# Kernel optimization log

Hardware: AMD Instinct MI355X
Metric: run time of the kernel (lower is better)

The kernel has to match this reference:

```python
import jax, jax.numpy as jnp
import numpy as np

N, E, D = 40000, 640000, 128
EPS = 1e-5


def _lin(k, out_d, in_d):
    s = 1.0 / np.sqrt(in_d)
    kw, kb = jax.random.split(k)
    W = jax.random.uniform(kw, (out_d, in_d), minval=-s, maxval=s, dtype=jnp.float32)
    b = jax.random.uniform(kb, (out_d,), minval=-s, maxval=s, dtype=jnp.float32)
    return W, b


def setup_inputs() -> dict:
    key = jax.random.key(0)
    kx, ke, k1, k2, k3, k4 = jax.random.split(key, 6)
    x = jax.random.normal(kx, (N, D), dtype=jnp.float32)
    edge_index = jax.random.randint(ke, (2, E), 0, N, dtype=jnp.int64)
    Wm1, bm1 = _lin(k1, D, D)
    Wm2, bm2 = _lin(k2, D, D)
    Wu1, bu1 = _lin(k3, D, 2 * D)
    Wu2, bu2 = _lin(k4, D, D)
    gamma = jnp.ones((D,), jnp.float32)
    beta = jnp.zeros((D,), jnp.float32)
    return dict(x=x, edge_index=edge_index, Wm1=Wm1, bm1=bm1, Wm2=Wm2, bm2=bm2,
                Wu1=Wu1, bu1=bu1, Wu2=Wu2, bu2=bu2, gamma=gamma, beta=beta)


def reference(x, edge_index, Wm1, bm1, Wm2, bm2, Wu1, bu1, Wu2, bu2, gamma, beta):
    num_nodes = x.shape[0]
    src, dst = edge_index[0], edge_index[1]
    # message MLP on gathered source features: (E, D)
    m = jax.nn.relu(x[src] @ Wm1.T + bm1) @ Wm2.T + bm2
    # scatter-mean via segment_sum + clamped count
    agg = jax.ops.segment_sum(m, dst, num_segments=num_nodes)
    cnt = jax.ops.segment_sum(jnp.ones((dst.shape[0],), m.dtype), dst, num_segments=num_nodes)
    agg = agg / jnp.clip(cnt, 1.0, None)[:, None]
    # update MLP on concat([x, agg]) -> (N, D); dropout is identity in eval
    comb = jnp.concatenate([x, agg], axis=-1)
    u = jax.nn.relu(comb @ Wu1.T + bu1) @ Wu2.T + bu2
    # residual + LayerNorm
    h = u + x
    mu = h.mean(-1, keepdims=True)
    var = ((h - mu) ** 2).mean(-1, keepdims=True)
    return (h - mu) / jnp.sqrt(var + EPS) * gamma + beta
```

## Files before the change

kernel.cpp:

```cpp
#include <hip/hip_runtime.h>

#define N_NODES 40000
#define N_EDGES 640000
#define DIM 128
#define PAD 64
#define NBLK_GEMM 313

typedef __bf16 bf16;
typedef __bf16 v8bf __attribute__((ext_vector_type(8)));
typedef __bf16 v4bf __attribute__((ext_vector_type(4)));
typedef float f32x4 __attribute__((ext_vector_type(4)));

#define MFMA(a, b, c) __builtin_amdgcn_mfma_f32_16x16x32_bf16(a, b, c, 0, 0, 0)

#define OFF_WM1 0
#define OFF_BM1 16384
#define OFF_WM2 16512
#define OFF_BM2 32896
#define OFF_WU1 33024
#define OFF_BU1 65792
#define OFF_WU2 65920
#define OFF_BU2 82304
#define OFF_GAM 82432
#define OFF_BET 82560
#define NPARAM  82688

__global__ __launch_bounds__(256) void front_kernel(
    const void* __restrict__ x, const void* __restrict__ ei,
    const void* p0, const void* p1, const void* p2, const void* p3,
    const void* p4, const void* p5, const void* p6, const void* p7,
    const void* p8, const void* p9,
    bf16* __restrict__ wp, bf16* __restrict__ xb,
    int* __restrict__ cnt, int* __restrict__ flags)
{
    __shared__ int sf[2];
    const int tid = threadIdx.x;
    const int gid = blockIdx.x * 256 + tid;
    const int gstride = gridDim.x * 256;

    if (tid == 0) { sf[0] = 0; sf[1] = 0; }
    __syncthreads();
    {
        const unsigned short* xh = (const unsigned short*)x;
        const unsigned int* eiw = (const unsigned int*)ei;
        int isf32 = 0; unsigned int orhi = 0;
        #pragma unroll
        for (int j = 0; j < 4; ++j) {
            unsigned short h = xh[2 * (tid + 256 * j)];
            if (((h >> 7) & 0xFF) >= 0xC0) isf32 = 1;
            orhi |= eiw[2 * (tid + 256 * j) + 1];
        }
        if (isf32) atomicOr(&sf[0], 1);
        if (orhi)  atomicOr(&sf[1], 1);
    }
    __syncthreads();
    const int f32m = sf[0];
    if (blockIdx.x == 0 && tid == 0) { flags[0] = f32m; flags[1] = sf[1] ? 0 : 1; }

    for (int i = gid; i < NPARAM; i += gstride) {
        const void* src; int base;
        if      (i < OFF_BM1) { src = p0; base = OFF_WM1; }
        else if (i < OFF_WM2) { src = p1; base = OFF_BM1; }
        else if (i < OFF_BM2) { src = p2; base = OFF_WM2; }
        else if (i < OFF_WU1) { src = p3; base = OFF_BM2; }
        else if (i < OFF_BU1) { src = p4; base = OFF_WU1; }
        else if (i < OFF_WU2) { src = p5; base = OFF_BU1; }
        else if (i < OFF_BU2) { src = p6; base = OFF_WU2; }
        else if (i < OFF_GAM) { src = p7; base = OFF_BU2; }
        else if (i < OFF_BET) { src = p8; base = OFF_GAM; }
        else                  { src = p9; base = OFF_BET; }
        int j = i - base;
        float v = f32m ? ((const float*)src)[j] : (float)((const bf16*)src)[j];
        wp[i] = (bf16)v;
    }
    {
        const int NT = N_NODES * DIM;
        if (f32m) {
            const float4* g = (const float4*)x;
            v4bf* o = (v4bf*)xb;
            for (int i = gid; i < NT / 4; i += gstride) {
                float4 v = g[i];
                v4bf t; t[0] = (bf16)v.x; t[1] = (bf16)v.y; t[2] = (bf16)v.z; t[3] = (bf16)v.w;
                o[i] = t;
            }
        } else {
            const uint4* g = (const uint4*)x;
            uint4* o = (uint4*)xb;
            for (int i = gid; i < NT / 8; i += gstride) o[i] = g[i];
        }
    }
    for (int i = gid; i < N_NODES; i += gstride) cnt[i] = 0;
}

__global__ __launch_bounds__(256) void scatter_kernel(const void* __restrict__ ei,
                                                      int* __restrict__ cnt,
                                                      int* __restrict__ padded,
                                                      const int* __restrict__ flags) {
    int e = blockIdx.x * 256 + threadIdx.x;
    if (e >= N_EDGES) return;
    int s, d;
    if (flags[1]) {
        const long long* p = (const long long*)ei;
        s = (int)p[e]; d = (int)p[N_EDGES + e];
    } else {
        const int* p = (const int*)ei;
        s = p[e]; d = p[N_EDGES + e];
    }
    int pos = atomicAdd(&cnt[d], 1);
    if (pos < PAD) padded[(d << 6) + pos] = s;
}

__global__ __launch_bounds__(256) void msg_kernel(const bf16* __restrict__ xb,
                                                  const bf16* __restrict__ wp,
                                                  bf16* __restrict__ y)
{
    __shared__ __align__(16) bf16 sc[4][32 * DIM];
    const int wave = threadIdx.x >> 6, lane = threadIdx.x & 63;
    const int l15 = lane & 15, quad = lane >> 4;
    const int row0 = (blockIdx.x * 4 + wave) * 32;
    bf16* s = sc[wave];
    const bf16* W1 = wp + OFF_WM1;
    const bf16* W2 = wp + OFF_WM2;

    const int ra = min(row0 + l15, N_NODES - 1);
    const int rb = min(row0 + 16 + l15, N_NODES - 1);

    f32x4 acc[2][8] = {};
    #pragma unroll
    for (int kt = 0; kt < 4; ++kt) {
        int k0 = kt * 32 + quad * 8;
        v8bf a0 = *(const v8bf*)&xb[(size_t)ra * DIM + k0];
        v8bf a1 = *(const v8bf*)&xb[(size_t)rb * DIM + k0];
        #pragma unroll
        for (int ct = 0; ct < 8; ++ct) {
            v8bf b = *(const v8bf*)&W1[(ct * 16 + l15) * DIM + k0];
            acc[0][ct] = MFMA(a0, b, acc[0][ct]);
            acc[1][ct] = MFMA(a1, b, acc[1][ct]);
        }
    }
    #pragma unroll
    for (int ct = 0; ct < 8; ++ct) {
        float bb = (float)wp[OFF_BM1 + ct * 16 + l15];
        int c8w = (ct << 1) | (l15 >> 3);
        #pragma unroll
        for (int i = 0; i < 2; ++i)
            #pragma unroll
            for (int r = 0; r < 4; ++r) {
                int row = i * 16 + quad * 4 + r;
                s[row * DIM + (((c8w ^ (row & 15)) << 3) | (l15 & 7))] =
                    (bf16)fmaxf(acc[i][ct][r] + bb, 0.f);
            }
    }
    f32x4 acc2[2][8] = {};
    #pragma unroll
    for (int kt = 0; kt < 4; ++kt) {
        int k0 = kt * 32 + quad * 8;
        int c8 = kt * 4 + quad;
        v8bf a0 = *(const v8bf*)&s[l15 * DIM + ((c8 ^ l15) << 3)];
        v8bf a1 = *(const v8bf*)&s[(16 + l15) * DIM + ((c8 ^ l15) << 3)];
        #pragma unroll
        for (int ct = 0; ct < 8; ++ct) {
            v8bf b = *(const v8bf*)&W2[(ct * 16 + l15) * DIM + k0];
            acc2[0][ct] = MFMA(a0, b, acc2[0][ct]);
            acc2[1][ct] = MFMA(a1, b, acc2[1][ct]);
        }
    }
    #pragma unroll
    for (int ct = 0; ct < 8; ++ct) {
        float bb = (float)wp[OFF_BM2 + ct * 16 + l15];
        #pragma unroll
        for (int i = 0; i < 2; ++i)
            #pragma unroll
            for (int r = 0; r < 4; ++r) {
                int grow = row0 + i * 16 + quad * 4 + r;
                if (grow < N_NODES)
                    y[(size_t)grow * DIM + ct * 16 + l15] = (bf16)(acc2[i][ct][r] + bb);
            }
    }
}

__global__ __launch_bounds__(256) void update_kernel(const bf16* __restrict__ xb,
                                                     const bf16* __restrict__ agg,
                                                     const bf16* __restrict__ wp,
                                                     const int* __restrict__ flags,
                                                     void* __restrict__ out)
{
    __shared__ __align__(16) bf16 sc[4][32 * DIM];
    const int wave = threadIdx.x >> 6, lane = threadIdx.x & 63;
    const int l15 = lane & 15, quad = lane >> 4;
    const int row0 = (blockIdx.x * 4 + wave) * 32;
    bf16* s = sc[wave];
    const bf16* W1 = wp + OFF_WU1;
    const bf16* W2 = wp + OFF_WU2;
    const int of32 = flags[0];

    const int ra = min(row0 + l15, N_NODES - 1);
    const int rb = min(row0 + 16 + l15, N_NODES - 1);

    f32x4 acc[2][8] = {};
    #pragma unroll
    for (int kt = 0; kt < 8; ++kt) {
        int k0 = kt * 32 + quad * 8;
        const bf16* A = (kt < 4) ? xb : agg;
        int ko = (kt < 4) ? k0 : (k0 - 128);
        v8bf a0 = *(const v8bf*)&A[(size_t)ra * DIM + ko];
        v8bf a1 = *(const v8bf*)&A[(size_t)rb * DIM + ko];
        #pragma unroll
        for (int ct = 0; ct < 8; ++ct) {
            v8bf b = *(const v8bf*)&W1[(ct * 16 + l15) * 256 + k0];
            acc[0][ct] = MFMA(a0, b, acc[0][ct]);
            acc[1][ct] = MFMA(a1, b, acc[1][ct]);
        }
    }
    #pragma unroll
    for (int ct = 0; ct < 8; ++ct) {
        float bb = (float)wp[OFF_BU1 + ct * 16 + l15];
        int c8w = (ct << 1) | (l15 >> 3);
        #pragma unroll
        for (int i = 0; i < 2; ++i)
            #pragma unroll
            for (int r = 0; r < 4; ++r) {
                int row = i * 16 + quad * 4 + r;
                s[row * DIM + (((c8w ^ (row & 15)) << 3) | (l15 & 7))] =
                    (bf16)fmaxf(acc[i][ct][r] + bb, 0.f);
            }
    }
    f32x4 acc2[2][8] = {};
    #pragma unroll
    for (int kt = 0; kt < 4; ++kt) {
        int k0 = kt * 32 + quad * 8;
        int c8 = kt * 4 + quad;
        v8bf a0 = *(const v8bf*)&s[l15 * DIM + ((c8 ^ l15) << 3)];
        v8bf a1 = *(const v8bf*)&s[(16 + l15) * DIM + ((c8 ^ l15) << 3)];
        #pragma unroll
        for (int ct = 0; ct < 8; ++ct) {
            v8bf b = *(const v8bf*)&W2[(ct * 16 + l15) * DIM + k0];
            acc2[0][ct] = MFMA(a0, b, acc2[0][ct]);
            acc2[1][ct] = MFMA(a1, b, acc2[1][ct]);
        }
    }

    float bu2c[8], gc[8], bc[8];
    #pragma unroll
    for (int ct = 0; ct < 8; ++ct) {
        int col = ct * 16 + l15;
        bu2c[ct] = (float)wp[OFF_BU2 + col];
        gc[ct]   = (float)wp[OFF_GAM + col];
        bc[ct]   = (float)wp[OFF_BET + col];
    }
    #pragma unroll
    for (int i = 0; i < 2; ++i) {
        #pragma unroll
        for (int r = 0; r < 4; ++r) {
            int grow = row0 + i * 16 + quad * 4 + r;
            int growc = min(grow, N_NODES - 1);
            float u[8], s1 = 0.f, s2 = 0.f;
            #pragma unroll
            for (int ct = 0; ct < 8; ++ct) {
                float v = acc2[i][ct][r] + bu2c[ct]
                        + (float)xb[(size_t)growc * DIM + ct * 16 + l15];
                u[ct] = v; s1 += v; s2 += v * v;
            }
            #pragma unroll
            for (int off = 1; off < 16; off <<= 1) {
                s1 += __shfl_xor(s1, off);
                s2 += __shfl_xor(s2, off);
            }
            float mean = s1 * (1.f / 128.f);
            float var  = s2 * (1.f / 128.f) - mean * mean;
            float rstd = rsqrtf(var + 1e-5f);
            if (grow < N_NODES) {
                if (of32) {
                    #pragma unroll
                    for (int ct = 0; ct < 8; ++ct)
                        ((float*)out)[(size_t)grow * DIM + ct * 16 + l15] =
                            (u[ct] - mean) * rstd * gc[ct] + bc[ct];
                } else {
                    #pragma unroll
                    for (int ct = 0; ct < 8; ++ct)
                        ((bf16*)out)[(size_t)grow * DIM + ct * 16 + l15] =
                            (bf16)((u[ct] - mean) * rstd * gc[ct] + bc[ct]);
                }
            }
        }
    }
}

__device__ __forceinline__ void accum8(float* s, uint4 v) {
    v8bf b = __builtin_bit_cast(v8bf, v);
    #pragma unroll
    for (int j = 0; j < 8; ++j) s[j] += (float)b[j];
}

__global__ __launch_bounds__(256) void agg_kernel(const bf16* __restrict__ y,
                                                  const int* __restrict__ padded,
                                                  const int* __restrict__ cnt,
                                                  bf16* __restrict__ agg) {
    const int node = (blockIdx.x << 2) + (threadIdx.x >> 6);
    const int lane = threadIdx.x & 63;
    const int slot = lane >> 4, c16 = lane & 15;
    const int c = min(cnt[node], PAD);
    const int beg = node << 6;
    const int end = beg + c;
    const uint4* yv = (const uint4*)y;

    float s0[8] = {}, s1[8] = {};
    int e = beg + slot;
    for (; e + 4 < end; e += 8) {
        int i0 = padded[e], i1 = padded[e + 4];
        uint4 v0 = yv[(size_t)i0 * 16 + c16];
        uint4 v1 = yv[(size_t)i1 * 16 + c16];
        accum8(s0, v0);
        accum8(s1, v1);
    }
    if (e < end) accum8(s0, yv[(size_t)padded[e] * 16 + c16]);

    float inv = 1.f / (float)(c > 0 ? c : 1);
    v8bf o;
    #pragma unroll
    for (int j = 0; j < 8; ++j) {
        float v = s0[j] + s1[j];
        v += __shfl_xor(v, 16);
        v += __shfl_xor(v, 32);
        o[j] = (bf16)(v * inv);
    }
    if (slot == 0)
        ((uint4*)agg)[(size_t)node * 16 + c16] = __builtin_bit_cast(uint4, o);
}

extern "C" void kernel_launch(void* const* d_in, const int* in_sizes, int n_in,
                              void* d_out, int out_size, void* d_ws, size_t ws_size,
                              hipStream_t stream) {
    const void* x  = d_in[0];
    const void* ei = d_in[1];

    char* ws = (char*)d_ws;
    size_t off = 0;
    auto alloc = [&](size_t bytes) {
        void* p = ws + off;
        off += (bytes + 255) & ~(size_t)255;
        return p;
    };
    bf16* y      = (bf16*)alloc((size_t)N_NODES * DIM * sizeof(bf16));
    bf16* agg    = (bf16*)alloc((size_t)N_NODES * DIM * sizeof(bf16));
    bf16* xb     = (bf16*)alloc((size_t)N_NODES * DIM * sizeof(bf16));
    bf16* wp     = (bf16*)alloc((size_t)NPARAM * sizeof(bf16));
    int*  cnt    = (int*)alloc(N_NODES * sizeof(int));
    int*  padded = (int*)alloc((size_t)N_NODES * PAD * sizeof(int));
    int*  flags  = (int*)alloc(256);

    front_kernel<<<1024, 256, 0, stream>>>(
        x, ei, d_in[2], d_in[3], d_in[4], d_in[5], d_in[6], d_in[7],
        d_in[8], d_in[9], d_in[10], d_in[11], wp, xb, cnt, flags);
    scatter_kernel<<<(N_EDGES + 255) / 256, 256, 0, stream>>>(ei, cnt, padded, flags);
    msg_kernel<<<NBLK_GEMM, 256, 0, stream>>>(xb, wp, y);
    agg_kernel<<<N_NODES / 4, 256, 0, stream>>>(y, padded, cnt, agg);
    update_kernel<<<NBLK_GEMM, 256, 0, stream>>>(xb, agg, wp, flags, d_out);
}
```

Measured before the change: 221.3 us.

## Fuse conversion into scatter, shrink GEMM tiles, use 16-bit neighbor indices

Merges the front conversion kernel into the scatter kernel, with each thread handling four edges for more atomic-level parallelism, and replaces the counter zeroing with a memset. Neighbor indices are stored as 16-bit values to halve padded-list traffic. The message and update GEMM kernels now give each wave 16 rows instead of 32, doubling the grid to 625 blocks for better occupancy at the cost of reusing weight loads less. Node ids up to 40000 fit in unsigned short, but the memset is now a separate launch and the tail bounds checks were removed because 40000 divides evenly.

Result: slower. 227.5 us (+2.8%).

```diff
diff --git a/kernel.cpp b/kernel.cpp
--- a/kernel.cpp
+++ b/kernel.cpp
@@ -4,7 +4,9 @@
 #define N_EDGES 640000
 #define DIM 128
 #define PAD 64
-#define NBLK_GEMM 313
+#define NBLK_GEMM 625
+#define SCAT_ILP 4
+#define SCAT_BLOCKS (N_EDGES / (256 * SCAT_ILP))
 
 typedef __bf16 bf16;
 typedef __bf16 v8bf __attribute__((ext_vector_type(8)));
@@ -25,38 +27,79 @@
 #define OFF_BET 82560
 #define NPARAM  82688
 
-__global__ __launch_bounds__(256) void front_kernel(
+__device__ __forceinline__ void detect(const void* x, const void* ei,
+                                       int* sf, int& f32m, int& i64m) {
+    const int tid = threadIdx.x;
+    if (tid == 0) { sf[0] = 0; sf[1] = 0; }
+    __syncthreads();
+    const unsigned short* xh = (const unsigned short*)x;
+    const unsigned int* eiw = (const unsigned int*)ei;
+    int isf32 = 0; unsigned int orhi = 0;
+    #pragma unroll
+    for (int j = 0; j < 4; ++j) {
+        unsigned short h = xh[2 * (tid + 256 * j)];
+        if (((h >> 7) & 0xFF) >= 0xC0) isf32 = 1;
+        orhi |= eiw[2 * (tid + 256 * j) + 1];
+    }
+    if (isf32) atomicOr(&sf[0], 1);
+    if (orhi)  atomicOr(&sf[1], 1);
+    __syncthreads();
+    f32m = sf[0];
+    i64m = sf[1] ? 0 : 1;
+}
+
+__global__ __launch_bounds__(256) void scatter_kernel(
     const void* __restrict__ x, const void* __restrict__ ei,
     const void* p0, const void* p1, const void* p2, const void* p3,
     const void* p4, const void* p5, const void* p6, const void* p7,
     const void* p8, const void* p9,
-    bf16* __restrict__ wp, bf16* __restrict__ xb,
-    int* __restrict__ cnt, int* __restrict__ flags)
+    int* __restrict__ cnt, unsigned short* __restrict__ padded,
+    bf16* __restrict__ xb, bf16* __restrict__ wp, int* __restrict__ flags)
 {
     __shared__ int sf[2];
-    const int tid = threadIdx.x;
-    const int gid = blockIdx.x * 256 + tid;
-    const int gstride = gridDim.x * 256;
-
-    if (tid == 0) { sf[0] = 0; sf[1] = 0; }
-    __syncthreads();
-    {
-        const unsigned short* xh = (const unsigned short*)x;
-        const unsigned int* eiw = (const unsigned int*)ei;
-        int isf32 = 0; unsigned int orhi = 0;
-        #pragma unroll
-        for (int j = 0; j < 4; ++j) {
-            unsigned short h = xh[2 * (tid + 256 * j)];
-            if (((h >> 7) & 0xFF) >= 0xC0) isf32 = 1;
-            orhi |= eiw[2 * (tid + 256 * j) + 1];
-        }
-        if (isf32) atomicOr(&sf[0], 1);
-        if (orhi)  atomicOr(&sf[1], 1);
-    }
-    __syncthreads();
-    const int f32m = sf[0];
-    if (blockIdx.x == 0 && tid == 0) { flags[0] = f32m; flags[1] = sf[1] ? 0 : 1; }
-
+    int f32m, i64m;
+    detect(x, ei, sf, f32m, i64m);
+    const int gid = blockIdx.x * 256 + threadIdx.x;
+    const int gstride = SCAT_BLOCKS * 256;
+    if (gid == 0) { flags[0] = f32m; flags[1] = i64m; }
+
+    int s[SCAT_ILP], d[SCAT_ILP];
+    if (i64m) {
+        const long long* p = (const long long*)ei;
+        #pragma unroll
+        for (int j = 0; j < SCAT_ILP; ++j) {
+            int e = gid + j * gstride;
+            s[j] = (int)p[e]; d[j] = (int)p[N_EDGES + e];
+        }
+    } else {
+        const int* p = (const int*)ei;
+        #pragma unroll
+        for (int j = 0; j < SCAT_ILP; ++j) {
+            int e = gid + j * gstride;
+            s[j] = p[e]; d[j] = p[N_EDGES + e];
+        }
+    }
+    int pos[SCAT_ILP];
+    #pragma unroll
+    for (int j = 0; j < SCAT_ILP; ++j) pos[j] = atomicAdd(&cnt[d[j]], 1);
+    #pragma unroll
+    for (int j = 0; j < SCAT_ILP; ++j)
+        if (pos[j] < PAD) padded[(d[j] << 6) + pos[j]] = (unsigned short)s[j];
+
+    const int NT = N_NODES * DIM;
+    if (f32m) {
+        const float4* g = (const float4*)x;
+        v4bf* o = (v4bf*)xb;
+        for (int i = gid; i < NT / 4; i += gstride) {
+            float4 v = g[i];
+            v4bf t; t[0] = (bf16)v.x; t[1] = (bf16)v.y; t[2] = (bf16)v.z; t[3] = (bf16)v.w;
+            o[i] = t;
+        }
+    } else {
+        const uint4* g = (const uint4*)x;
+        uint4* o = (uint4*)xb;
+        for (int i = gid; i < NT / 8; i += gstride) o[i] = g[i];
+    }
     for (int i = gid; i < NPARAM; i += gstride) {
         const void* src; int base;
         if      (i < OFF_BM1) { src = p0; base = OFF_WM1; }
@@ -73,69 +116,28 @@
         float v = f32m ? ((const float*)src)[j] : (float)((const bf16*)src)[j];
         wp[i] = (bf16)v;
     }
-    {
-        const int NT = N_NODES * DIM;
-        if (f32m) {
-            const float4* g = (const float4*)x;
-            v4bf* o = (v4bf*)xb;
-            for (int i = gid; i < NT / 4; i += gstride) {
-                float4 v = g[i];
-                v4bf t; t[0] = (bf16)v.x; t[1] = (bf16)v.y; t[2] = (bf16)v.z; t[3] = (bf16)v.w;
-                o[i] = t;
-            }
-        } else {
-            const uint4* g = (const uint4*)x;
-            uint4* o = (uint4*)xb;
-            for (int i = gid; i < NT / 8; i += gstride) o[i] = g[i];
-        }
-    }
-    for (int i = gid; i < N_NODES; i += gstride) cnt[i] = 0;
-}
-
-__global__ __launch_bounds__(256) void scatter_kernel(const void* __restrict__ ei,
-                                                      int* __restrict__ cnt,
-                                                      int* __restrict__ padded,
-                                                      const int* __restrict__ flags) {
-    int e = blockIdx.x * 256 + threadIdx.x;
-    if (e >= N_EDGES) return;
-    int s, d;
-    if (flags[1]) {
-        const long long* p = (const long long*)ei;
-        s = (int)p[e]; d = (int)p[N_EDGES + e];
-    } else {
-        const int* p = (const int*)ei;
-        s = p[e]; d = p[N_EDGES + e];
-    }
-    int pos = atomicAdd(&cnt[d], 1);
-    if (pos < PAD) padded[(d << 6) + pos] = s;
 }
 
 __global__ __launch_bounds__(256) void msg_kernel(const bf16* __restrict__ xb,
                                                   const bf16* __restrict__ wp,
                                                   bf16* __restrict__ y)
 {
-    __shared__ __align__(16) bf16 sc[4][32 * DIM];
+    __shared__ __align__(16) bf16 sc[4][16 * DIM];
     const int wave = threadIdx.x >> 6, lane = threadIdx.x & 63;
     const int l15 = lane & 15, quad = lane >> 4;
-    const int row0 = (blockIdx.x * 4 + wave) * 32;
+    const int row0 = (blockIdx.x * 4 + wave) * 16;
     bf16* s = sc[wave];
-    const bf16* W1 = wp + OFF_WM1;
-    const bf16* W2 = wp + OFF_WM2;
-
-    const int ra = min(row0 + l15, N_NODES - 1);
-    const int rb = min(row0 + 16 + l15, N_NODES - 1);
-
-    f32x4 acc[2][8] = {};
+    const size_t ra = (size_t)(row0 + l15) * DIM;
+
+    f32x4 acc[8] = {};
     #pragma unroll
     for (int kt = 0; kt < 4; ++kt) {
         int k0 = kt * 32 + quad * 8;
-        v8bf a0 = *(const v8bf*)&xb[(size_t)ra * DIM + k0];
-        v8bf a1 = *(const v8bf*)&xb[(size_t)rb * DIM + k0];
-        #pragma unroll
-        for (int ct = 0; ct < 8; ++ct) {
-            v8bf b = *(const v8bf*)&W1[(ct * 16 + l15) * DIM + k0];
-            acc[0][ct] = MFMA(a0, b, acc[0][ct]);
-            acc[1][ct] = MFMA(a1, b, acc[1][ct]);
+        v8bf a0 = *(const v8bf*)&xb[ra + k0];
+        #pragma unroll
+        for (int ct = 0; ct < 8; ++ct) {
+            v8bf b = *(const v8bf*)&wp[OFF_WM1 + (size_t)(ct * 16 + l15) * DIM + k0];
+            acc[ct] = MFMA(a0, b, acc[ct]);
         }
     }
     #pragma unroll
@@ -143,145 +145,31 @@
         float bb = (float)wp[OFF_BM1 + ct * 16 + l15];
         int c8w = (ct << 1) | (l15 >> 3);
         #pragma unroll
-        for (int i = 0; i < 2; ++i)
-            #pragma unroll
-            for (int r = 0; r < 4; ++r) {
-                int row = i * 16 + quad * 4 + r;
-                s[row * DIM + (((c8w ^ (row & 15)) << 3) | (l15 & 7))] =
-                    (bf16)fmaxf(acc[i][ct][r] + bb, 0.f);
-            }
-    }
-    f32x4 acc2[2][8] = {};
+        for (int r = 0; r < 4; ++r) {
+            int row = quad * 4 + r;
+            s[row * DIM + (((c8w ^ row) << 3) | (l15 & 7))] =
+                (bf16)fmaxf(acc[ct][r] + bb, 0.f);
+        }
+    }
+    f32x4 acc2[8] = {};
     #pragma unroll
     for (int kt = 0; kt < 4; ++kt) {
         int k0 = kt * 32 + quad * 8;
         int c8 = kt * 4 + quad;
         v8bf a0 = *(const v8bf*)&s[l15 * DIM + ((c8 ^ l15) << 3)];
-        v8bf a1 = *(const v8bf*)&s[(16 + l15) * DIM + ((c8 ^ l15) << 3)];
-        #pragma unroll
-        for (int ct = 0; ct < 8; ++ct) {
-            v8bf b = *(const v8bf*)&W2[(ct * 16 + l15) * DIM + k0];
-            acc2[0][ct] = MFMA(a0, b, acc2[0][ct]);
-            acc2[1][ct] = MFMA(a1, b, acc2[1][ct]);
+        #pragma unroll
+        for (int ct = 0; ct < 8; ++ct) {
+            v8bf b = *(const v8bf*)&wp[OFF_WM2 + (size_t)(ct * 16 + l15) * DIM + k0];
+            acc2[ct] = MFMA(a0, b, acc2[ct]);
         }
     }
     #pragma unroll
     for (int ct = 0; ct < 8; ++ct) {
         float bb = (float)wp[OFF_BM2 + ct * 16 + l15];
         #pragma unroll
-        for (int i = 0; i < 2; ++i)
-            #pragma unroll
-            for (int r = 0; r < 4; ++r) {
-                int grow = row0 + i * 16 + quad * 4 + r;
-                if (grow < N_NODES)
-                    y[(size_t)grow * DIM + ct * 16 + l15] = (bf16)(acc2[i][ct][r] + bb);
-            }
-    }
-}
-
-__global__ __launch_bounds__(256) void update_kernel(const bf16* __restrict__ xb,
-                                                     const bf16* __restrict__ agg,
-                                                     const bf16* __restrict__ wp,
-                                                     const int* __restrict__ flags,
-                                                     void* __restrict__ out)
-{
-    __shared__ __align__(16) bf16 sc[4][32 * DIM];
-    const int wave = threadIdx.x >> 6, lane = threadIdx.x & 63;
-    const int l15 = lane & 15, quad = lane >> 4;
-    const int row0 = (blockIdx.x * 4 + wave) * 32;
-    bf16* s = sc[wave];
-    const bf16* W1 = wp + OFF_WU1;
-    const bf16* W2 = wp + OFF_WU2;
-    const int of32 = flags[0];
-
-    const int ra = min(row0 + l15, N_NODES - 1);
-    const int rb = min(row0 + 16 + l15, N_NODES - 1);
-
-    f32x4 acc[2][8] = {};
-    #pragma unroll
-    for (int kt = 0; kt < 8; ++kt) {
-        int k0 = kt * 32 + quad * 8;
-        const bf16* A = (kt < 4) ? xb : agg;
-        int ko = (kt < 4) ? k0 : (k0 - 128);
-        v8bf a0 = *(const v8bf*)&A[(size_t)ra * DIM + ko];
-        v8bf a1 = *(const v8bf*)&A[(size_t)rb * DIM + ko];
-        #pragma unroll
-        for (int ct = 0; ct < 8; ++ct) {
-            v8bf b = *(const v8bf*)&W1[(ct * 16 + l15) * 256 + k0];
-            acc[0][ct] = MFMA(a0, b, acc[0][ct]);
-            acc[1][ct] = MFMA(a1, b, acc[1][ct]);
-        }
-    }
-    #pragma unroll
-    for (int ct = 0; ct < 8; ++ct) {
-        float bb = (float)wp[OFF_BU1 + ct * 16 + l15];
-        int c8w = (ct << 1) | (l15 >> 3);
-        #pragma unroll
-        for (int i = 0; i < 2; ++i)
-            #pragma unroll
-            for (int r = 0; r < 4; ++r) {
-                int row = i * 16 + quad * 4 + r;
-                s[row * DIM + (((c8w ^ (row & 15)) << 3) | (l15 & 7))] =
-                    (bf16)fmaxf(acc[i][ct][r] + bb, 0.f);
-            }
-    }
-    f32x4 acc2[2][8] = {};
-    #pragma unroll
-    for (int kt = 0; kt < 4; ++kt) {
-        int k0 = kt * 32 + quad * 8;
-        int c8 = kt * 4 + quad;
-        v8bf a0 = *(const v8bf*)&s[l15 * DIM + ((c8 ^ l15) << 3)];
-        v8bf a1 = *(const v8bf*)&s[(16 + l15) * DIM + ((c8 ^ l15) << 3)];
-        #pragma unroll
-        for (int ct = 0; ct < 8; ++ct) {
-            v8bf b = *(const v8bf*)&W2[(ct * 16 + l15) * DIM + k0];
-            acc2[0][ct] = MFMA(a0, b, acc2[0][ct]);
-            acc2[1][ct] = MFMA(a1, b, acc2[1][ct]);
-        }
-    }
-
-    float bu2c[8], gc[8], bc[8];
-    #pragma unroll
-    for (int ct = 0; ct < 8; ++ct) {
-        int col = ct * 16 + l15;
-        bu2c[ct] = (float)wp[OFF_BU2 + col];
-        gc[ct]   = (float)wp[OFF_GAM + col];
-        bc[ct]   = (float)wp[OFF_BET + col];
-    }
-    #pragma unroll
-    for (int i = 0; i < 2; ++i) {
-        #pragma unroll
         for (int r = 0; r < 4; ++r) {
-            int grow = row0 + i * 16 + quad * 4 + r;
-            int growc = min(grow, N_NODES - 1);
-            float u[8], s1 = 0.f, s2 = 0.f;
-            #pragma unroll
-            for (int ct = 0; ct < 8; ++ct) {
-                float v = acc2[i][ct][r] + bu2c[ct]
-                        + (float)xb[(size_t)growc * DIM + ct * 16 + l15];
-                u[ct] = v; s1 += v; s2 += v * v;
-            }
-            #pragma unroll
-            for (int off = 1; off < 16; off <<= 1) {
-                s1 += __shfl_xor(s1, off);
-                s2 += __shfl_xor(s2, off);
-            }
-            float mean = s1 * (1.f / 128.f);
-            float var  = s2 * (1.f / 128.f) - mean * mean;
-            float rstd = rsqrtf(var + 1e-5f);
-            if (grow < N_NODES) {
-                if (of32) {
-                    #pragma unroll
-                    for (int ct = 0; ct < 8; ++ct)
-                        ((float*)out)[(size_t)grow * DIM + ct * 16 + l15] =
-                            (u[ct] - mean) * rstd * gc[ct] + bc[ct];
-                } else {
-                    #pragma unroll
-                    for (int ct = 0; ct < 8; ++ct)
-                        ((bf16*)out)[(size_t)grow * DIM + ct * 16 + l15] =
-                            (bf16)((u[ct] - mean) * rstd * gc[ct] + bc[ct]);
-                }
-            }
+            int grow = row0 + quad * 4 + r;
+            y[(size_t)grow * DIM + ct * 16 + l15] = (bf16)(acc2[ct][r] + bb);
         }
     }
 }
@@ -293,7 +181,7 @@
 }
 
 __global__ __launch_bounds__(256) void agg_kernel(const bf16* __restrict__ y,
-                                                  const int* __restrict__ padded,
+                                                  const unsigned short* __restrict__ padded,
                                                   const int* __restrict__ cnt,
                                                   bf16* __restrict__ agg) {
     const int node = (blockIdx.x << 2) + (threadIdx.x >> 6);
@@ -328,6 +216,95 @@
         ((uint4*)agg)[(size_t)node * 16 + c16] = __builtin_bit_cast(uint4, o);
 }
 
+__global__ __launch_bounds__(256) void update_kernel(
+    const bf16* __restrict__ xb, const bf16* __restrict__ agg,
+    const bf16* __restrict__ wp, const int* __restrict__ flags,
+    void* __restrict__ out)
+{
+    __shared__ __align__(16) bf16 sc[4][16 * DIM];
+    const int wave = threadIdx.x >> 6, lane = threadIdx.x & 63;
+    const int l15 = lane & 15, quad = lane >> 4;
+    const int row0 = (blockIdx.x * 4 + wave) * 16;
+    bf16* s = sc[wave];
+    const size_t ra = (size_t)(row0 + l15) * DIM;
+    const int of32 = flags[0];
+
+    f32x4 acc[8] = {};
+    #pragma unroll
+    for (int kt = 0; kt < 8; ++kt) {
+        int k0 = kt * 32 + quad * 8;
+        v8bf a0 = (kt < 4) ? *(const v8bf*)&xb[ra + k0]
+                           : *(const v8bf*)&agg[ra + (k0 - 128)];
+        #pragma unroll
+        for (int ct = 0; ct < 8; ++ct) {
+            v8bf b = *(const v8bf*)&wp[OFF_WU1 + (size_t)(ct * 16 + l15) * 256 + k0];
+            acc[ct] = MFMA(a0, b, acc[ct]);
+        }
+    }
+    #pragma unroll
+    for (int ct = 0; ct < 8; ++ct) {
+        float bb = (float)wp[OFF_BU1 + ct * 16 + l15];
+        int c8w = (ct << 1) | (l15 >> 3);
+        #pragma unroll
+        for (int r = 0; r < 4; ++r) {
+            int row = quad * 4 + r;
+            s[row * DIM + (((c8w ^ row) << 3) | (l15 & 7))] =
+                (bf16)fmaxf(acc[ct][r] + bb, 0.f);
+        }
+    }
+    f32x4 acc2[8] = {};
+    #pragma unroll
+    for (int kt = 0; kt < 4; ++kt) {
+        int k0 = kt * 32 + quad * 8;
+        int c8 = kt * 4 + quad;
+        v8bf a0 = *(const v8bf*)&s[l15 * DIM + ((c8 ^ l15) << 3)];
+        #pragma unroll
+        for (int ct = 0; ct < 8; ++ct) {
+            v8bf b = *(const v8bf*)&wp[OFF_WU2 + (size_t)(ct * 16 + l15) * DIM + k0];
+            acc2[ct] = MFMA(a0, b, acc2[ct]);
+        }
+    }
+
+    float bu2c[8], gc[8], bc[8];
+    #pragma unroll
+    for (int ct = 0; ct < 8; ++ct) {
+        int col = ct * 16 + l15;
+        bu2c[ct] = (float)wp[OFF_BU2 + col];
+        gc[ct]   = (float)wp[OFF_GAM + col];
+        bc[ct]   = (float)wp[OFF_BET + col];
+    }
+    #pragma unroll
+    for (int r = 0; r < 4; ++r) {
+        int grow = row0 + quad * 4 + r;
+        float u[8], s1 = 0.f, s2 = 0.f;
+        #pragma unroll
+        for (int ct = 0; ct < 8; ++ct) {
+            float v = acc2[ct][r] + bu2c[ct]
+                    + (float)xb[(size_t)grow * DIM + ct * 16 + l15];
+            u[ct] = v; s1 += v; s2 += v * v;
+        }
+        #pragma unroll
+        for (int off = 1; off < 16; off <<= 1) {
+            s1 += __shfl_xor(s1, off);
+            s2 += __shfl_xor(s2, off);
+        }
+        float mean = s1 * (1.f / 128.f);
+        float var  = s2 * (1.f / 128.f) - mean * mean;
+        float rstd = rsqrtf(var + 1e-5f);
+        if (of32) {
+            #pragma unroll
+            for (int ct = 0; ct < 8; ++ct)
+                ((float*)out)[(size_t)grow * DIM + ct * 16 + l15] =
+                    (u[ct] - mean) * rstd * gc[ct] + bc[ct];
+        } else {
+            #pragma unroll
+            for (int ct = 0; ct < 8; ++ct)
+                ((bf16*)out)[(size_t)grow * DIM + ct * 16 + l15] =
+                    (bf16)((u[ct] - mean) * rstd * gc[ct] + bc[ct]);
+        }
+    }
+}
+
 extern "C" void kernel_launch(void* const* d_in, const int* in_sizes, int n_in,
                               void* d_out, int out_size, void* d_ws, size_t ws_size,
                               hipStream_t stream) {
@@ -341,18 +318,20 @@
         off += (bytes + 255) & ~(size_t)255;
         return p;
     };
-    bf16* y      = (bf16*)alloc((size_t)N_NODES * DIM * sizeof(bf16));
-    bf16* agg    = (bf16*)alloc((size_t)N_NODES * DIM * sizeof(bf16));
-    bf16* xb     = (bf16*)alloc((size_t)N_NODES * DIM * sizeof(bf16));
-    bf16* wp     = (bf16*)alloc((size_t)NPARAM * sizeof(bf16));
-    int*  cnt    = (int*)alloc(N_NODES * sizeof(int));
-    int*  padded = (int*)alloc((size_t)N_NODES * PAD * sizeof(int));
-    int*  flags  = (int*)alloc(256);
-
-    front_kernel<<<1024, 256, 0, stream>>>(
+    bf16* y   = (bf16*)alloc((size_t)N_NODES * DIM * sizeof(bf16));
+    bf16* agg = (bf16*)alloc((size_t)N_NODES * DIM * sizeof(bf16));
+    bf16* xb  = (bf16*)alloc((size_t)N_NODES * DIM * sizeof(bf16));
+    bf16* wp  = (bf16*)alloc((size_t)NPARAM * sizeof(bf16));
+    int*  cnt = (int*)alloc(N_NODES * sizeof(int));
+    unsigned short* padded =
+        (unsigned short*)alloc((size_t)N_NODES * PAD * sizeof(unsigned short));
+    int* flags = (int*)alloc(256);
+
+    hipMemsetAsync(cnt, 0, N_NODES * sizeof(int), stream);
+
+    scatter_kernel<<<SCAT_BLOCKS, 256, 0, stream>>>(
         x, ei, d_in[2], d_in[3], d_in[4], d_in[5], d_in[6], d_in[7],
-        d_in[8], d_in[9], d_in[10], d_in[11], wp, xb, cnt, flags);
-    scatter_kernel<<<(N_EDGES + 255) / 256, 256, 0, stream>>>(ei, cnt, padded, flags);
+        d_in[8], d_in[9], d_in[10], d_in[11], cnt, padded, xb, wp, flags);
     msg_kernel<<<NBLK_GEMM, 256, 0, stream>>>(xb, wp, y);
     agg_kernel<<<N_NODES / 4, 256, 0, stream>>>(y, padded, cnt, agg);
     update_kernel<<<NBLK_GEMM, 256, 0, stream>>>(xb, agg, wp, flags, d_out);
```
